# Optimization experiments

Measured on AMD Instinct MI355X. Metric: run time of the kernel, lower is better.

The kernel has to match this reference:

```python
import jax, jax.numpy as jnp
import numpy as np

DIM = 384
NUM_HEADS = 12
WS = 8            # window_size
SS = 4            # shift_size
HEAD_DIM = DIM // NUM_HEADS
SCALE = HEAD_DIM ** -0.5
N = WS * WS       # tokens per window
EPS = 1e-5
MLP_HIDDEN = 4 * DIM

# relative position index (static, matches torch buffer construction)
_coords = np.stack(np.meshgrid(np.arange(WS), np.arange(WS), indexing='ij')).reshape(2, -1)
_rel = (_coords[:, :, None] - _coords[:, None, :]).transpose(1, 2, 0)  # [N,N,2]
_rel[..., 0] += WS - 1
_rel[..., 1] += WS - 1
_rel[..., 0] *= 2 * WS - 1
RPI = jnp.asarray(_rel.sum(-1))  # [N,N] int


def layer_norm(x, g, b):
    m = x.mean(-1, keepdims=True)
    v = ((x - m) ** 2).mean(-1, keepdims=True)
    return (x - m) / jnp.sqrt(v + EPS) * g + b


def window_partition(x):
    B, Hh, Ww, C = x.shape
    x = x.reshape(B, Hh // WS, WS, Ww // WS, WS, C).transpose(0, 1, 3, 2, 4, 5)
    return x.reshape(-1, WS, WS, C)


def window_reverse(w, Hh, Ww):
    B = w.shape[0] // ((Hh // WS) * (Ww // WS))
    x = w.reshape(B, Hh // WS, Ww // WS, WS, WS, -1).transpose(0, 1, 3, 2, 4, 5)
    return x.reshape(B, Hh, Ww, -1)


def attention_mask(Hp, Wp):
    # region id along each axis: 0 = [0, Hp-WS), 1 = [Hp-WS, Hp-SS), 2 = [Hp-SS, Hp)
    h_id = np.zeros(Hp, np.int32); h_id[Hp - WS:Hp - SS] = 1; h_id[Hp - SS:] = 2
    w_id = np.zeros(Wp, np.int32); w_id[Wp - WS:Wp - SS] = 1; w_id[Wp - SS:] = 2
    cnt = h_id[:, None] * 3 + w_id[None, :]                      # [Hp, Wp]
    img = jnp.asarray(cnt, jnp.float32).reshape(1, Hp, Wp, 1)
    mw = window_partition(img).reshape(-1, N)                    # [nW, N]
    am = mw[:, None, :] - mw[:, :, None]                         # [nW, N, N]
    return jnp.where(am != 0, jnp.float32(-100.0), jnp.float32(0.0))


def setup_inputs() -> dict:
    key = jax.random.key(0)
    ks = jax.random.split(key, 8)
    B, H, W = 32, 64, 64
    std = 0.02
    return {
        'x': jax.random.normal(ks[0], (B, H * W, DIM), jnp.float32),
        'qkv_w': jax.random.normal(ks[1], (DIM, 3 * DIM), jnp.float32) * std,
        'qkv_b': jnp.zeros((3 * DIM,), jnp.float32),
        'proj_w': jax.random.normal(ks[2], (DIM, DIM), jnp.float32) * std,
        'proj_b': jnp.zeros((DIM,), jnp.float32),
        'rpb_table': jax.random.normal(ks[3], ((2 * WS - 1) * (2 * WS - 1), NUM_HEADS), jnp.float32) * std,
        'n1_g': jnp.ones((DIM,), jnp.float32), 'n1_b': jnp.zeros((DIM,), jnp.float32),
        'n2_g': jnp.ones((DIM,), jnp.float32), 'n2_b': jnp.zeros((DIM,), jnp.float32),
        'fc1_w': jax.random.normal(ks[4], (DIM, MLP_HIDDEN), jnp.float32) * std,
        'fc1_b': jnp.zeros((MLP_HIDDEN,), jnp.float32),
        'fc2_w': jax.random.normal(ks[5], (MLP_HIDDEN, DIM), jnp.float32) * std,
        'fc2_b': jnp.zeros((DIM,), jnp.float32),
        'H': 64, 'W': 64,
    }


def reference(x, qkv_w, qkv_b, proj_w, proj_b, rpb_table, n1_g, n1_b, n2_g, n2_b,
              fc1_w, fc1_b, fc2_w, fc2_b, H, W):
    B, L, C = x.shape
    shortcut = x
    h = layer_norm(x, n1_g, n1_b).reshape(B, H, W, C)
    pad_r = (WS - W % WS) % WS
    pad_b = (WS - H % WS) % WS
    if pad_r or pad_b:
        h = jnp.pad(h, ((0, 0), (0, pad_b), (0, pad_r), (0, 0)))
    Hp, Wp = H + pad_b, W + pad_r
    shifted = jnp.roll(h, shift=(-SS, -SS), axis=(1, 2))
    xw = window_partition(shifted).reshape(-1, N, C)             # [B_, N, C]
    B_ = xw.shape[0]

    qkv = (xw @ qkv_w + qkv_b).reshape(B_, N, 3, NUM_HEADS, HEAD_DIM)
    q = qkv[:, :, 0].transpose(0, 2, 1, 3) * SCALE               # [B_, h, N, d]
    k = qkv[:, :, 1].transpose(0, 2, 1, 3)
    v = qkv[:, :, 2].transpose(0, 2, 1, 3)

    attn = jnp.einsum('bhnd,bhmd->bhnm', q, k)                   # [B_, h, N, N]
    bias = rpb_table[RPI].transpose(2, 0, 1)                     # [h, N, N]
    attn = attn + bias[None]

    mask = attention_mask(Hp, Wp)                                # [nW, N, N]
    nW = mask.shape[0]
    attn = attn.reshape(B_ // nW, nW, NUM_HEADS, N, N) + mask[None, :, None]
    attn = jax.nn.softmax(attn.reshape(B_, NUM_HEADS, N, N), axis=-1)

    out = jnp.einsum('bhnm,bhmd->bhnd', attn, v)
    out = out.transpose(0, 2, 1, 3).reshape(B_, N, C)
    out = out @ proj_w + proj_b

    out = window_reverse(out.reshape(-1, WS, WS, C), Hp, Wp)
    out = jnp.roll(out, shift=(SS, SS), axis=(1, 2))
    out = out[:, :H, :W, :].reshape(B, H * W, C)

    x = shortcut + out
    h2 = layer_norm(x, n2_g, n2_b)
    mlp = jax.nn.gelu(h2 @ fc1_w + fc1_b, approximate=False) @ fc2_w + fc2_b
    return x + mlp
```

## Files before the change

### kernel.cpp

```cpp
#include <hip/hip_runtime.h>
#include <math.h>


#define ROWS_TOTAL 131072
#define NWIN_TOTAL 2048

typedef __attribute__((ext_vector_type(8))) __bf16 bf16x8;
typedef __attribute__((ext_vector_type(4))) float f32x4;
typedef __attribute__((ext_vector_type(8))) unsigned short ushort8;

__device__ __forceinline__ unsigned short f2bf(float f) {
  unsigned u = __builtin_bit_cast(unsigned, f);
  u = (u + 0x7fffu + ((u >> 16) & 1u)) >> 16;
  return (unsigned short)u;
}
__device__ __forceinline__ float bf2f(unsigned short u) {
  return __builtin_bit_cast(float, (unsigned)u << 16);
}

__device__ __forceinline__ void gload16(const void* g, void* l) {
  __builtin_amdgcn_global_load_lds(
      (const __attribute__((address_space(1))) unsigned int*)g,
      (__attribute__((address_space(3))) unsigned int*)l, 16, 0, 0);
}

__device__ __forceinline__ int gather_row(int win, int t) {
  int b = win >> 6, wi = (win >> 3) & 7, wj = win & 7;
  int gi = (wi * 8 + (t >> 3) + 4) & 63;
  int gj = (wj * 8 + (t & 7) + 4) & 63;
  return (b << 12) + (gi << 6) + gj;
}

__device__ __forceinline__ float gelu_f(float v) {
  float x = v * 0.70710678118654752f;
  float ax = fabsf(x);
  float t = 1.f / (1.f + 0.3275911f * ax);
  float poly =
      t * (0.254829592f +
           t * (-0.284496736f +
                t * (1.421413741f + t * (-1.453152027f + t * 1.061405429f))));
  float er = 1.f - poly * __expf(-x * x);
  er = copysignf(er, x);
  return 0.5f * v * (1.f + er);
}

#define LGK0() asm volatile("s_waitcnt lgkmcnt(0)" ::: "memory")
#define VM4() asm volatile("s_waitcnt vmcnt(4)" ::: "memory")
#define VM0() asm volatile("s_waitcnt vmcnt(0)" ::: "memory")
#define SCB() __builtin_amdgcn_sched_barrier(0)
#define BARR() __builtin_amdgcn_s_barrier()
#define PRIO1() __builtin_amdgcn_s_setprio(1)
#define PRIO0() __builtin_amdgcn_s_setprio(0)

#define STGA_(buf_, kt_, c_)                                          \
  gload16(aSrcC[c_] + (size_t)(kt_) * 64,                             \
          (char*)As + (buf_) * 32768 + (c_) * 8192 + w * 1024)
#define STGB_(buf_, kt_, c_)                                          \
  gload16(bSrcC[c_] + (size_t)(kt_) * 64,                             \
          (char*)Bs + (buf_) * 24576 + (c_) * 8192 + w * 1024)

#define MM3(mi_, a_, bs_)                                             \
  { acc[mi_][0] = __builtin_amdgcn_mfma_f32_16x16x32_bf16(            \
        a_, bs_[0], acc[mi_][0], 0, 0, 0);                            \
    acc[mi_][1] = __builtin_amdgcn_mfma_f32_16x16x32_bf16(            \
        a_, bs_[1], acc[mi_][1], 0, 0, 0);                            \
    acc[mi_][2] = __builtin_amdgcn_mfma_f32_16x16x32_bf16(            \
        a_, bs_[2], acc[mi_][2], 0, 0, 0); }

#define GEMM_DECLS()                                                  \
  f32x4 acc[8][3];                                                    \
  _Pragma("unroll") for (int i_ = 0; i_ < 8; ++i_)                    \
  _Pragma("unroll") for (int j_ = 0; j_ < 3; ++j_)                    \
      acc[i_][j_] = (f32x4)(0.f);                                     \
  const int sl0 = ((hi) ^ (lr & 7)) * 8;                              \
  const int sl1 = ((4 + hi) ^ (lr & 7)) * 8;                          \
  const int aB0 = (wr * 128 + lr) * 64 + sl0;                         \
  const int aB1 = (wr * 128 + lr) * 64 + sl1;                         \
  const int bB0 = (wc * 48 + lr) * 64 + sl0;                          \
  const int bB1 = (wc * 48 + lr) * 64 + sl1;

#define GEMM_CORE(NT_)                                                \
  {                                                                   \
    STGA_(0, 0, 0); STGA_(0, 0, 1); STGA_(0, 0, 2); STGA_(0, 0, 3);   \
    STGB_(0, 0, 0); STGB_(0, 0, 1); STGB_(0, 0, 2);                   \
    STGA_(1, 1, 0); STGA_(1, 1, 1); STGA_(1, 1, 2); STGA_(1, 1, 3);   \
    VM4(); SCB(); BARR(); SCB();                                      \
    int curA = 0;                                                     \
    for (int t = 0; t < (NT_); ++t) {                                 \
      const int curB = t & 1;                                         \
      const ushort* AsC = (const ushort*)As + curA * 16384;           \
      const ushort* BsC = (const ushort*)Bs + curB * 12288;           \
      if (t + 1 < (NT_)) {                                            \
        STGB_(curB ^ 1, t + 1, 0);                                    \
        STGB_(curB ^ 1, t + 1, 1);                                    \
        STGB_(curB ^ 1, t + 1, 2);                                    \
      }                                                               \
      SCB();                                                          \
      bf16x8 av0, av1, av2, av3, bv0[3], bv1[3];                      \
      bv0[0] = *(const bf16x8*)(BsC + bB0);                           \
      bv0[1] = *(const bf16x8*)(BsC + bB0 + 1024);                    \
      bv0[2] = *(const bf16x8*)(BsC + bB0 + 2048);                    \
      bv1[0] = *(const bf16x8*)(BsC + bB1);                           \
      bv1[1] = *(const bf16x8*)(BsC + bB1 + 1024);                    \
      bv1[2] = *(const bf16x8*)(BsC + bB1 + 2048);                    \
      av0 = *(const bf16x8*)(AsC + aB0);                              \
      av1 = *(const bf16x8*)(AsC + aB0 + 1024);                       \
      av2 = *(const bf16x8*)(AsC + aB0 + 2048);                       \
      av3 = *(const bf16x8*)(AsC + aB0 + 3072);                       \
      LGK0(); SCB();                                                  \
      PRIO1();                                                        \
      MM3(0, av0, bv0); MM3(1, av1, bv0);                             \
      MM3(2, av2, bv0); MM3(3, av3, bv0);                             \
      PRIO0(); SCB();                                                 \
      av0 = *(const bf16x8*)(AsC + aB1);                              \
      av1 = *(const bf16x8*)(AsC + aB1 + 1024);                       \
      av2 = *(const bf16x8*)(AsC + aB1 + 2048);                       \
      av3 = *(const bf16x8*)(AsC + aB1 + 3072);                       \
      LGK0(); SCB();                                                  \
      PRIO1();                                                        \
      MM3(0, av0, bv1); MM3(1, av1, bv1);                             \
      MM3(2, av2, bv1); MM3(3, av3, bv1);                             \
      PRIO0(); SCB();                                                 \
      if (t + 2 < (NT_)) {                                            \
        int nbA = curA + 2; if (nbA >= 3) nbA -= 3;                   \
        STGA_(nbA, t + 2, 0); STGA_(nbA, t + 2, 1);                   \
        STGA_(nbA, t + 2, 2); STGA_(nbA, t + 2, 3);                   \
      }                                                               \
      SCB();                                                          \
      av0 = *(const bf16x8*)(AsC + aB0 + 4096);                       \
      av1 = *(const bf16x8*)(AsC + aB0 + 5120);                       \
      av2 = *(const bf16x8*)(AsC + aB0 + 6144);                       \
      av3 = *(const bf16x8*)(AsC + aB0 + 7168);                       \
      LGK0(); SCB();                                                  \
      PRIO1();                                                        \
      MM3(4, av0, bv0); MM3(5, av1, bv0);                             \
      MM3(6, av2, bv0); MM3(7, av3, bv0);                             \
      PRIO0(); SCB();                                                 \
      av0 = *(const bf16x8*)(AsC + aB1 + 4096);                       \
      av1 = *(const bf16x8*)(AsC + aB1 + 5120);                       \
      av2 = *(const bf16x8*)(AsC + aB1 + 6144);                       \
      av3 = *(const bf16x8*)(AsC + aB1 + 7168);                       \
      LGK0(); SCB();                                                  \
      PRIO1();                                                        \
      MM3(4, av0, bv1); MM3(5, av1, bv1);                             \
      MM3(6, av2, bv1); MM3(7, av3, bv1);                             \
      PRIO0();                                                        \
      if (t + 2 < (NT_)) { VM4(); SCB(); BARR(); SCB(); }             \
      else if (t + 1 < (NT_)) { VM0(); SCB(); BARR(); SCB(); }        \
      ++curA; if (curA == 3) curA = 0;                                \
    }                                                                 \
  }

#define GRID_SWZ(NP_)                                                 \
  int p, bm;                                                          \
  {                                                                   \
    int lin = blockIdx.y * (NP_) + blockIdx.x;                        \
    if ((gridDim.y & 7) == 0) {                                       \
      int xcd = lin & 7, q = lin >> 3;                                \
      p = q % (NP_); bm = (q / (NP_)) * 8 + xcd;                      \
    } else { p = blockIdx.x; bm = blockIdx.y; }                       \
  }

__global__ __launch_bounds__(256) void wprep_k(
    const float* __restrict__ qkvw, const float* __restrict__ projw,
    const float* __restrict__ fc1w, const float* __restrict__ fc2w,
    ushort* __restrict__ wq, ushort* __restrict__ wp,
    ushort* __restrict__ w1, ushort* __restrict__ w2) {
  int gid = blockIdx.x * 256 + threadIdx.x;
  const int S1 = 1152 * 384;
  const int S2 = S1 + 384 * 384;
  const int S3 = S2 + 1536 * 384;
  const int S4 = S3 + 384 * 1536;
  if (gid < S1) {
    int n = gid / 384, k = gid - n * 384;
    wq[gid] = f2bf(qkvw[(size_t)k * 1152 + n]);
  } else if (gid < S2) {
    int i = gid - S1, n = i / 384, k = i - n * 384;
    wp[i] = f2bf(projw[(size_t)k * 384 + n]);
  } else if (gid < S3) {
    int i = gid - S2, n = i / 384, k = i - n * 384;
    w1[i] = f2bf(fc1w[(size_t)k * 1536 + n]);
  } else if (gid < S4) {
    int i = gid - S3, n = i / 1536, k = i - n * 1536;
    w2[i] = f2bf(fc2w[(size_t)k * 384 + n]);
  }
}

__global__ __launch_bounds__(256) void ln_fused_k(
    const float* __restrict__ x, const float* __restrict__ g,
    const float* __restrict__ b, ushort* __restrict__ o) {
  int wid = threadIdx.x >> 6, lane = threadIdx.x & 63;
  int row = (blockIdx.x << 2) + wid;
  const float* p = x + (size_t)row * 384;
  float2 v[3];
  float s = 0.f, ss = 0.f;
#pragma unroll
  for (int c = 0; c < 3; ++c) {
    v[c] = *(const float2*)(p + lane * 2 + c * 128);
    s += v[c].x + v[c].y;
    ss += v[c].x * v[c].x + v[c].y * v[c].y;
  }
#pragma unroll
  for (int off = 1; off < 64; off <<= 1) {
    s += __shfl_xor(s, off);
    ss += __shfl_xor(ss, off);
  }
  float m = s * (1.f / 384.f);
  float r = rsqrtf(ss * (1.f / 384.f) - m * m + 1e-5f);
  ushort* op = o + (size_t)row * 384;
#pragma unroll
  for (int c = 0; c < 3; ++c) {
    float2 gg = *(const float2*)(g + lane * 2 + c * 128);
    float2 bb = *(const float2*)(b + lane * 2 + c * 128);
    union { ushort u[2]; unsigned w; } pk;
    pk.u[0] = f2bf((v[c].x - m) * r * gg.x + bb.x);
    pk.u[1] = f2bf((v[c].y - m) * r * gg.y + bb.y);
    *(unsigned*)(op + lane * 2 + c * 128) = pk.w;
  }
}

__global__ __launch_bounds__(512) void qkv_mfma_k(
    const ushort* __restrict__ xln, const ushort* __restrict__ wq,
    const float* __restrict__ qkvb, ushort* __restrict__ qd,
    ushort* __restrict__ kd, ushort* __restrict__ vd, int wc0) {
  __shared__ __align__(16) ushort As[3][16384];
  __shared__ __align__(16) ushort Bs[2][12288];
  const int tid = threadIdx.x;
  const int w = tid >> 6, lane = tid & 63;
  const int wr = w >> 2, wc = w & 3;
  const int lr = lane & 15, hi = lane >> 4;
  GRID_SWZ(6);
  const int n0 = p * 192;
  const int sg = ((tid & 7) ^ ((tid >> 3) & 7)) * 8;
  const ushort* aSrcC[4];
  const ushort* bSrcC[3];
#pragma unroll
  for (int c = 0; c < 4; ++c)
    aSrcC[c] =
        xln + (size_t)gather_row(wc0 + bm * 4 + c, tid >> 3) * 384 + sg;
#pragma unroll
  for (int c = 0; c < 3; ++c)
    bSrcC[c] = wq + (size_t)(n0 + c * 64 + (tid >> 3)) * 384 + sg;
  GEMM_DECLS();
  GEMM_CORE(6);
  const float scale = 0.17677669529663687f;
#pragma unroll
  for (int mi = 0; mi < 8; ++mi) {
#pragma unroll
    for (int r = 0; r < 4; ++r) {
      int rr = wr * 128 + mi * 16 + (hi << 2) + r;
      int w_rel = bm * 4 + (rr >> 6), t = rr & 63;
#pragma unroll
      for (int nj = 0; nj < 3; ++nj) {
        int nc = n0 + wc * 48 + nj * 16 + lr;
        float v = acc[mi][nj][r] + qkvb[nc];
        int qi = nc / 384, rem = nc - qi * 384;
        int hh = rem >> 5, d = rem & 31;
        ushort* base = (qi == 0) ? qd : (qi == 1 ? kd : vd);
        if (qi == 0) v *= scale;
        base[(((size_t)w_rel * 12 + hh) << 11) + (t << 5) + d] = f2bf(v);
      }
    }
  }
}

__global__ __launch_bounds__(128) void attn_k(
    const ushort* __restrict__ q, const ushort* __restrict__ k,
    const ushort* __restrict__ v, const float* __restrict__ rpb,
    ushort* __restrict__ ao, int wc0) {
  __shared__ __align__(16) float kbuf[2][64][32];
  __shared__ __align__(16) float vbuf[2][64][32];
  __shared__ float bias[2][232];
  __shared__ int region[64];
  const int tid = threadIdx.x;
  const int wid = tid >> 6, lane = tid & 63;
  const int w = blockIdx.x, win = wc0 + w;
  const int head = blockIdx.y * 2 + wid;
  if (tid < 64) {
    int wi = (win >> 3) & 7, wj = win & 7;
    int pi = wi * 8 + (tid >> 3), pj = wj * 8 + (tid & 7);
    int ri = pi < 56 ? 0 : (pi < 60 ? 1 : 2);
    int rj = pj < 56 ? 0 : (pj < 60 ? 1 : 2);
    region[tid] = ri * 3 + rj;
  }
  const size_t hb = ((size_t)w * 12 + head) * 2048;
  const ushort* kp = k + hb;
  const ushort* vp = v + hb;
#pragma unroll
  for (int s = 0; s < 4; ++s) {
    int f = s * 64 + lane;
    int r = f >> 2, c = (f & 3) * 8;
    ushort8 ku = *(const ushort8*)(kp + r * 32 + c);
    ushort8 vu = *(const ushort8*)(vp + r * 32 + c);
#pragma unroll
    for (int j = 0; j < 8; ++j) {
      kbuf[wid][r][c + j] = bf2f(ku[j]);
      vbuf[wid][r][c + j] = bf2f(vu[j]);
    }
  }
  for (int s = lane; s < 225; s += 64) bias[wid][s] = rpb[s * 12 + head];
  __syncthreads();
  const int i = lane;
  float qr[32];
  const ushort* qp = q + hb + (i << 5);
#pragma unroll
  for (int c = 0; c < 4; ++c) {
    ushort8 qu = *(const ushort8*)(qp + c * 8);
#pragma unroll
    for (int j = 0; j < 8; ++j) qr[c * 8 + j] = bf2f(qu[j]);
  }
  const int yi = i >> 3, xi = i & 7, regi = region[i];
  float sc[64];
  float mx = -3.0e38f;
#pragma unroll
  for (int j = 0; j < 64; ++j) {
    float a = 0.f;
#pragma unroll
    for (int c = 0; c < 32; c += 4) {
      float4 kv = *(float4*)&kbuf[wid][j][c];
      a = fmaf(qr[c], kv.x, a);
      a = fmaf(qr[c + 1], kv.y, a);
      a = fmaf(qr[c + 2], kv.z, a);
      a = fmaf(qr[c + 3], kv.w, a);
    }
    int dy = yi - (j >> 3) + 7, dx = xi - (j & 7) + 7;
    a += bias[wid][dy * 15 + dx];
    if (region[j] != regi) a -= 100.f;
    sc[j] = a;
    mx = fmaxf(mx, a);
  }
  float sum = 0.f;
#pragma unroll
  for (int j = 0; j < 64; ++j) {
    float e = __expf(sc[j] - mx);
    sc[j] = e;
    sum += e;
  }
  const float inv = 1.f / sum;
  float o[32];
#pragma unroll
  for (int c = 0; c < 32; ++c) o[c] = 0.f;
#pragma unroll
  for (int j = 0; j < 64; ++j) {
    float p = sc[j];
#pragma unroll
    for (int c = 0; c < 32; c += 4) {
      float4 vv = *(float4*)&vbuf[wid][j][c];
      o[c] = fmaf(p, vv.x, o[c]);
      o[c + 1] = fmaf(p, vv.y, o[c + 1]);
      o[c + 2] = fmaf(p, vv.z, o[c + 2]);
      o[c + 3] = fmaf(p, vv.w, o[c + 3]);
    }
  }
  ushort* op = ao + ((size_t)(w * 64 + i)) * 384 + (head << 5);
#pragma unroll
  for (int c = 0; c < 32; c += 8) {
    ushort8 pk;
#pragma unroll
    for (int j2 = 0; j2 < 8; ++j2) pk[j2] = f2bf(o[c + j2] * inv);
    *(ushort8*)(op + c) = pk;
  }
}

__global__ __launch_bounds__(512) void proj_mfma_k(
    const ushort* __restrict__ ao, const ushort* __restrict__ wp,
    const float* __restrict__ pb, const float* __restrict__ x,
    float* __restrict__ x2, int wc0) {
  __shared__ __align__(16) ushort As[3][16384];
  __shared__ __align__(16) ushort Bs[2][12288];
  const int tid = threadIdx.x;
  const int w = tid >> 6, lane = tid & 63;
  const int wr = w >> 2, wc = w & 3;
  const int lr = lane & 15, hi = lane >> 4;
  GRID_SWZ(2);
  const int n0 = p * 192;
  const int sg = ((tid & 7) ^ ((tid >> 3) & 7)) * 8;
  const ushort* aSrcC[4];
  const ushort* bSrcC[3];
#pragma unroll
  for (int c = 0; c < 4; ++c)
    aSrcC[c] = ao + (size_t)(bm * 256 + c * 64 + (tid >> 3)) * 384 + sg;
#pragma unroll
  for (int c = 0; c < 3; ++c)
    bSrcC[c] = wp + (size_t)(n0 + c * 64 + (tid >> 3)) * 384 + sg;
  GEMM_DECLS();
  GEMM_CORE(6);
#pragma unroll
  for (int mi = 0; mi < 8; ++mi) {
#pragma unroll
    for (int r = 0; r < 4; ++r) {
      int rr = wr * 128 + mi * 16 + (hi << 2) + r;
      int gl = bm * 256 + rr;
      int gr = gather_row(wc0 + (gl >> 6), gl & 63);
#pragma unroll
      for (int nj = 0; nj < 3; ++nj) {
        int nc = n0 + wc * 48 + nj * 16 + lr;
        size_t idx = (size_t)gr * 384 + nc;
        x2[idx] = acc[mi][nj][r] + pb[nc] + x[idx];
      }
    }
  }
}

__global__ __launch_bounds__(512) void fc1_mfma_k(
    const ushort* __restrict__ x2ln, const ushort* __restrict__ w1,
    const float* __restrict__ fb, ushort* __restrict__ hm, int row0) {
  __shared__ __align__(16) ushort As[3][16384];
  __shared__ __align__(16) ushort Bs[2][12288];
  const int tid = threadIdx.x;
  const int w = tid >> 6, lane = tid & 63;
  const int wr = w >> 2, wc = w & 3;
  const int lr = lane & 15, hi = lane >> 4;
  GRID_SWZ(8);
  const int n0 = p * 192;
  const int sg = ((tid & 7) ^ ((tid >> 3) & 7)) * 8;
  const ushort* aSrcC[4];
  const ushort* bSrcC[3];
#pragma unroll
  for (int c = 0; c < 4; ++c)
    aSrcC[c] =
        x2ln + (size_t)(row0 + bm * 256 + c * 64 + (tid >> 3)) * 384 + sg;
#pragma unroll
  for (int c = 0; c < 3; ++c)
    bSrcC[c] = w1 + (size_t)(n0 + c * 64 + (tid >> 3)) * 384 + sg;
  GEMM_DECLS();
  GEMM_CORE(6);
#pragma unroll
  for (int mi = 0; mi < 8; ++mi) {
#pragma unroll
    for (int r = 0; r < 4; ++r) {
      int rr = wr * 128 + mi * 16 + (hi << 2) + r;
      size_t lrow = (size_t)(bm * 256 + rr);
#pragma unroll
      for (int nj = 0; nj < 3; ++nj) {
        int nc = n0 + wc * 48 + nj * 16 + lr;
        float v = gelu_f(acc[mi][nj][r] + fb[nc]);
        hm[lrow * 1536 + nc] = f2bf(v);
      }
    }
  }
}

__global__ __launch_bounds__(512) void fc2_mfma_k(
    const ushort* __restrict__ hm, const ushort* __restrict__ w2,
    const float* __restrict__ fb, float* __restrict__ out, int row0) {
  __shared__ __align__(16) ushort As[3][16384];
  __shared__ __align__(16) ushort Bs[2][12288];
  const int tid = threadIdx.x;
  const int w = tid >> 6, lane = tid & 63;
  const int wr = w >> 2, wc = w & 3;
  const int lr = lane & 15, hi = lane >> 4;
  GRID_SWZ(2);
  const int n0 = p * 192;
  const int sg = ((tid & 7) ^ ((tid >> 3) & 7)) * 8;
  const ushort* aSrcC[4];
  const ushort* bSrcC[3];
#pragma unroll
  for (int c = 0; c < 4; ++c)
    aSrcC[c] = hm + (size_t)(bm * 256 + c * 64 + (tid >> 3)) * 1536 + sg;
#pragma unroll
  for (int c = 0; c < 3; ++c)
    bSrcC[c] = w2 + (size_t)(n0 + c * 64 + (tid >> 3)) * 1536 + sg;
  GEMM_DECLS();
  GEMM_CORE(24);
#pragma unroll
  for (int mi = 0; mi < 8; ++mi) {
#pragma unroll
    for (int r = 0; r < 4; ++r) {
      int rr = wr * 128 + mi * 16 + (hi << 2) + r;
      size_t grow = (size_t)(row0 + bm * 256 + rr);
#pragma unroll
      for (int nj = 0; nj < 3; ++nj) {
        int nc = n0 + wc * 48 + nj * 16 + lr;
        size_t idx = grow * 384 + nc;
        out[idx] = out[idx] + acc[mi][nj][r] + fb[nc];
      }
    }
  }
}

extern "C" void kernel_launch(void* const* d_in, const int* in_sizes, int n_in,
                              void* d_out, int out_size, void* d_ws, size_t ws_size,
                              hipStream_t stream) {
  const float* x = (const float*)d_in[0];
  const float* qkv_w = (const float*)d_in[1];
  const float* qkv_b = (const float*)d_in[2];
  const float* proj_w = (const float*)d_in[3];
  const float* proj_b = (const float*)d_in[4];
  const float* rpb = (const float*)d_in[5];
  const float* n1g = (const float*)d_in[6];
  const float* n1b = (const float*)d_in[7];
  const float* n2g = (const float*)d_in[8];
  const float* n2b = (const float*)d_in[9];
  const float* fc1w = (const float*)d_in[10];
  const float* fc1b = (const float*)d_in[11];
  const float* fc2w = (const float*)d_in[12];
  const float* fc2b = (const float*)d_in[13];
  float* out = (float*)d_out;
  char* ws = (char*)d_ws;

  ushort* wq = (ushort*)ws;
  ushort* wp = wq + 442368;
  ushort* w1 = wp + 147456;
  ushort* w2 = w1 + 589824;
  ushort* xln = (ushort*)(ws + 3538944);
  char* scratch = ws + 3538944 + 100663296;
  size_t base = 3538944 + 100663296;
  size_t ssz = (ws_size > base) ? ws_size - base : 0;

  wprep_k<<<6912, 256, 0, stream>>>(qkv_w, proj_w, fc1w, fc2w, wq, wp, w1, w2);
  ln_fused_k<<<ROWS_TOTAL / 4, 256, 0, stream>>>(x, n1g, n1b, xln);

  const size_t perwin = 196608;
  int nwc = (int)(ssz / perwin);
  if (nwc > NWIN_TOTAL) nwc = NWIN_TOTAL;
  nwc &= ~31;
  if (nwc < 32) nwc = 32;
  ushort* qd = (ushort*)scratch;
  ushort* kd = qd + (size_t)nwc * 24576;
  ushort* vd = kd + (size_t)nwc * 24576;
  ushort* ao = vd + (size_t)nwc * 24576;
  for (int wc0 = 0; wc0 < NWIN_TOTAL; wc0 += nwc) {
    int nw = (NWIN_TOTAL - wc0 < nwc) ? (NWIN_TOTAL - wc0) : nwc;
    qkv_mfma_k<<<dim3(6, nw / 4), 512, 0, stream>>>(xln, wq, qkv_b, qd, kd,
                                                    vd, wc0);
    attn_k<<<dim3(nw, 6), 128, 0, stream>>>(qd, kd, vd, rpb, ao, wc0);
    proj_mfma_k<<<dim3(2, nw / 4), 512, 0, stream>>>(ao, wp, proj_b, x, out,
                                                     wc0);
  }

  ln_fused_k<<<ROWS_TOTAL / 4, 256, 0, stream>>>(out, n2g, n2b, xln);
  const size_t pergrp = 786432;
  int ngc = (int)(ssz / pergrp);
  if (ngc > 512) ngc = 512;
  ngc &= ~7;
  if (ngc < 8) ngc = 8;
  ushort* hm = (ushort*)scratch;
  for (int g0 = 0; g0 < 512; g0 += ngc) {
    int ng = (512 - g0 < ngc) ? (512 - g0) : ngc;
    fc1_mfma_k<<<dim3(8, ng), 512, 0, stream>>>(xln, w1, fc1b, hm, g0 * 256);
    fc2_mfma_k<<<dim3(2, ng), 512, 0, stream>>>(hm, w2, fc2b, out, g0 * 256);
  }
}
```

Baseline: 1.373 ms.

## Simplify GEMM inner loop, pack QKV row-major, cap chunk sizes, add launch bounds

The hand-scheduled GEMM inner loop, with its sched barriers, priority switches and explicit lgkmcnt waits, is replaced by plain unrolled loops, leaving instruction scheduling to the compiler. The QKV output is stored as one row-major [rows,1152] buffer, and attention reads K, V and Q by strided column offsets instead of separate per-head contiguous arrays. Window and MLP group chunk caps shrink to 256 and 128 so intermediates stay more cache-resident, and the GEMM kernels get launch_bounds(512,2) to target two blocks per CU. These changes risk losing the tuned LDS/MFMA overlap and make attention loads less coalesced, while the occupancy hint may force register spills.

```diff
diff --git a/kernel.cpp b/kernel.cpp
--- a/kernel.cpp
+++ b/kernel.cpp
@@ -44,13 +44,9 @@
   return 0.5f * v * (1.f + er);
 }
 
-#define LGK0() asm volatile("s_waitcnt lgkmcnt(0)" ::: "memory")
 #define VM4() asm volatile("s_waitcnt vmcnt(4)" ::: "memory")
 #define VM0() asm volatile("s_waitcnt vmcnt(0)" ::: "memory")
-#define SCB() __builtin_amdgcn_sched_barrier(0)
-#define BARR() __builtin_amdgcn_s_barrier()
-#define PRIO1() __builtin_amdgcn_s_setprio(1)
-#define PRIO0() __builtin_amdgcn_s_setprio(0)
+#define ABAR() asm volatile("s_barrier" ::: "memory")
 
 #define STGA_(buf_, kt_, c_)                                          \
   gload16(aSrcC[c_] + (size_t)(kt_) * 64,                             \
@@ -58,14 +54,6 @@
 #define STGB_(buf_, kt_, c_)                                          \
   gload16(bSrcC[c_] + (size_t)(kt_) * 64,                             \
           (char*)Bs + (buf_) * 24576 + (c_) * 8192 + w * 1024)
-
-#define MM3(mi_, a_, bs_)                                             \
-  { acc[mi_][0] = __builtin_amdgcn_mfma_f32_16x16x32_bf16(            \
-        a_, bs_[0], acc[mi_][0], 0, 0, 0);                            \
-    acc[mi_][1] = __builtin_amdgcn_mfma_f32_16x16x32_bf16(            \
-        a_, bs_[1], acc[mi_][1], 0, 0, 0);                            \
-    acc[mi_][2] = __builtin_amdgcn_mfma_f32_16x16x32_bf16(            \
-        a_, bs_[2], acc[mi_][2], 0, 0, 0); }
 
 #define GEMM_DECLS()                                                  \
   f32x4 acc[8][3];                                                    \
@@ -84,7 +72,7 @@
     STGA_(0, 0, 0); STGA_(0, 0, 1); STGA_(0, 0, 2); STGA_(0, 0, 3);   \
     STGB_(0, 0, 0); STGB_(0, 0, 1); STGB_(0, 0, 2);                   \
     STGA_(1, 1, 0); STGA_(1, 1, 1); STGA_(1, 1, 2); STGA_(1, 1, 3);   \
-    VM4(); SCB(); BARR(); SCB();                                      \
+    VM4(); ABAR();                                                    \
     int curA = 0;                                                     \
     for (int t = 0; t < (NT_); ++t) {                                 \
       const int curB = t & 1;                                         \
@@ -95,58 +83,28 @@
         STGB_(curB ^ 1, t + 1, 1);                                    \
         STGB_(curB ^ 1, t + 1, 2);                                    \
       }                                                               \
-      SCB();                                                          \
-      bf16x8 av0, av1, av2, av3, bv0[3], bv1[3];                      \
-      bv0[0] = *(const bf16x8*)(BsC + bB0);                           \
-      bv0[1] = *(const bf16x8*)(BsC + bB0 + 1024);                    \
-      bv0[2] = *(const bf16x8*)(BsC + bB0 + 2048);                    \
-      bv1[0] = *(const bf16x8*)(BsC + bB1);                           \
-      bv1[1] = *(const bf16x8*)(BsC + bB1 + 1024);                    \
-      bv1[2] = *(const bf16x8*)(BsC + bB1 + 2048);                    \
-      av0 = *(const bf16x8*)(AsC + aB0);                              \
-      av1 = *(const bf16x8*)(AsC + aB0 + 1024);                       \
-      av2 = *(const bf16x8*)(AsC + aB0 + 2048);                       \
-      av3 = *(const bf16x8*)(AsC + aB0 + 3072);                       \
-      LGK0(); SCB();                                                  \
-      PRIO1();                                                        \
-      MM3(0, av0, bv0); MM3(1, av1, bv0);                             \
-      MM3(2, av2, bv0); MM3(3, av3, bv0);                             \
-      PRIO0(); SCB();                                                 \
-      av0 = *(const bf16x8*)(AsC + aB1);                              \
-      av1 = *(const bf16x8*)(AsC + aB1 + 1024);                       \
-      av2 = *(const bf16x8*)(AsC + aB1 + 2048);                       \
-      av3 = *(const bf16x8*)(AsC + aB1 + 3072);                       \
-      LGK0(); SCB();                                                  \
-      PRIO1();                                                        \
-      MM3(0, av0, bv1); MM3(1, av1, bv1);                             \
-      MM3(2, av2, bv1); MM3(3, av3, bv1);                             \
-      PRIO0(); SCB();                                                 \
       if (t + 2 < (NT_)) {                                            \
         int nbA = curA + 2; if (nbA >= 3) nbA -= 3;                   \
         STGA_(nbA, t + 2, 0); STGA_(nbA, t + 2, 1);                   \
         STGA_(nbA, t + 2, 2); STGA_(nbA, t + 2, 3);                   \
       }                                                               \
-      SCB();                                                          \
-      av0 = *(const bf16x8*)(AsC + aB0 + 4096);                       \
-      av1 = *(const bf16x8*)(AsC + aB0 + 5120);                       \
-      av2 = *(const bf16x8*)(AsC + aB0 + 6144);                       \
-      av3 = *(const bf16x8*)(AsC + aB0 + 7168);                       \
-      LGK0(); SCB();                                                  \
-      PRIO1();                                                        \
-      MM3(4, av0, bv0); MM3(5, av1, bv0);                             \
-      MM3(6, av2, bv0); MM3(7, av3, bv0);                             \
-      PRIO0(); SCB();                                                 \
-      av0 = *(const bf16x8*)(AsC + aB1 + 4096);                       \
-      av1 = *(const bf16x8*)(AsC + aB1 + 5120);                       \
-      av2 = *(const bf16x8*)(AsC + aB1 + 6144);                       \
-      av3 = *(const bf16x8*)(AsC + aB1 + 7168);                       \
-      LGK0(); SCB();                                                  \
-      PRIO1();                                                        \
-      MM3(4, av0, bv1); MM3(5, av1, bv1);                             \
-      MM3(6, av2, bv1); MM3(7, av3, bv1);                             \
-      PRIO0();                                                        \
-      if (t + 2 < (NT_)) { VM4(); SCB(); BARR(); SCB(); }             \
-      else if (t + 1 < (NT_)) { VM0(); SCB(); BARR(); SCB(); }        \
+      bf16x8 bv0[3], bv1[3];                                          \
+      _Pragma("unroll") for (int nj = 0; nj < 3; ++nj) {              \
+        bv0[nj] = *(const bf16x8*)(BsC + bB0 + nj * 1024);            \
+        bv1[nj] = *(const bf16x8*)(BsC + bB1 + nj * 1024);            \
+      }                                                               \
+      _Pragma("unroll") for (int mi = 0; mi < 8; ++mi) {              \
+        bf16x8 a0 = *(const bf16x8*)(AsC + aB0 + mi * 1024);          \
+        bf16x8 a1 = *(const bf16x8*)(AsC + aB1 + mi * 1024);          \
+        _Pragma("unroll") for (int nj = 0; nj < 3; ++nj) {            \
+          acc[mi][nj] = __builtin_amdgcn_mfma_f32_16x16x32_bf16(      \
+              a0, bv0[nj], acc[mi][nj], 0, 0, 0);                     \
+          acc[mi][nj] = __builtin_amdgcn_mfma_f32_16x16x32_bf16(      \
+              a1, bv1[nj], acc[mi][nj], 0, 0, 0);                     \
+        }                                                             \
+      }                                                               \
+      if (t + 2 < (NT_)) { VM4(); ABAR(); }                           \
+      else if (t + 1 < (NT_)) { VM0(); ABAR(); }                      \
       ++curA; if (curA == 3) curA = 0;                                \
     }                                                                 \
   }
@@ -219,10 +177,9 @@
   }
 }
 
-__global__ __launch_bounds__(512) void qkv_mfma_k(
+__global__ __launch_bounds__(512, 2) void qkv_mfma_k(
     const ushort* __restrict__ xln, const ushort* __restrict__ wq,
-    const float* __restrict__ qkvb, ushort* __restrict__ qd,
-    ushort* __restrict__ kd, ushort* __restrict__ vd, int wc0) {
+    const float* __restrict__ qkvb, ushort* __restrict__ qkvd, int wc0) {
   __shared__ __align__(16) ushort As[3][16384];
   __shared__ __align__(16) ushort Bs[2][12288];
   const int tid = threadIdx.x;
@@ -249,24 +206,20 @@
 #pragma unroll
     for (int r = 0; r < 4; ++r) {
       int rr = wr * 128 + mi * 16 + (hi << 2) + r;
-      int w_rel = bm * 4 + (rr >> 6), t = rr & 63;
+      size_t row = (size_t)(bm * 256 + rr);
 #pragma unroll
       for (int nj = 0; nj < 3; ++nj) {
         int nc = n0 + wc * 48 + nj * 16 + lr;
         float v = acc[mi][nj][r] + qkvb[nc];
-        int qi = nc / 384, rem = nc - qi * 384;
-        int hh = rem >> 5, d = rem & 31;
-        ushort* base = (qi == 0) ? qd : (qi == 1 ? kd : vd);
-        if (qi == 0) v *= scale;
-        base[(((size_t)w_rel * 12 + hh) << 11) + (t << 5) + d] = f2bf(v);
+        if (nc < 384) v *= scale;
+        qkvd[row * 1152 + nc] = f2bf(v);
       }
     }
   }
 }
 
 __global__ __launch_bounds__(128) void attn_k(
-    const ushort* __restrict__ q, const ushort* __restrict__ k,
-    const ushort* __restrict__ v, const float* __restrict__ rpb,
+    const ushort* __restrict__ qkv, const float* __restrict__ rpb,
     ushort* __restrict__ ao, int wc0) {
   __shared__ __align__(16) float kbuf[2][64][32];
   __shared__ __align__(16) float vbuf[2][64][32];
@@ -283,15 +236,14 @@
     int rj = pj < 56 ? 0 : (pj < 60 ? 1 : 2);
     region[tid] = ri * 3 + rj;
   }
-  const size_t hb = ((size_t)w * 12 + head) * 2048;
-  const ushort* kp = k + hb;
-  const ushort* vp = v + hb;
+  const ushort* base = qkv + (size_t)(w * 64) * 1152;
+  const int kcol = 384 + head * 32, vcol = 768 + head * 32;
 #pragma unroll
   for (int s = 0; s < 4; ++s) {
     int f = s * 64 + lane;
     int r = f >> 2, c = (f & 3) * 8;
-    ushort8 ku = *(const ushort8*)(kp + r * 32 + c);
-    ushort8 vu = *(const ushort8*)(vp + r * 32 + c);
+    ushort8 ku = *(const ushort8*)(base + (size_t)r * 1152 + kcol + c);
+    ushort8 vu = *(const ushort8*)(base + (size_t)r * 1152 + vcol + c);
 #pragma unroll
     for (int j = 0; j < 8; ++j) {
       kbuf[wid][r][c + j] = bf2f(ku[j]);
@@ -302,7 +254,7 @@
   __syncthreads();
   const int i = lane;
   float qr[32];
-  const ushort* qp = q + hb + (i << 5);
+  const ushort* qp = base + (size_t)i * 1152 + head * 32;
 #pragma unroll
   for (int c = 0; c < 4; ++c) {
     ushort8 qu = *(const ushort8*)(qp + c * 8);
@@ -362,7 +314,7 @@
   }
 }
 
-__global__ __launch_bounds__(512) void proj_mfma_k(
+__global__ __launch_bounds__(512, 2) void proj_mfma_k(
     const ushort* __restrict__ ao, const ushort* __restrict__ wp,
     const float* __restrict__ pb, const float* __restrict__ x,
     float* __restrict__ x2, int wc0) {
@@ -402,7 +354,7 @@
   }
 }
 
-__global__ __launch_bounds__(512) void fc1_mfma_k(
+__global__ __launch_bounds__(512, 2) void fc1_mfma_k(
     const ushort* __restrict__ x2ln, const ushort* __restrict__ w1,
     const float* __restrict__ fb, ushort* __restrict__ hm, int row0) {
   __shared__ __align__(16) ushort As[3][16384];
@@ -441,7 +393,7 @@
   }
 }
 
-__global__ __launch_bounds__(512) void fc2_mfma_k(
+__global__ __launch_bounds__(512, 2) void fc2_mfma_k(
     const ushort* __restrict__ hm, const ushort* __restrict__ w2,
     const float* __restrict__ fb, float* __restrict__ out, int row0) {
   __shared__ __align__(16) ushort As[3][16384];
@@ -513,18 +465,15 @@
 
   const size_t perwin = 196608;
   int nwc = (int)(ssz / perwin);
-  if (nwc > NWIN_TOTAL) nwc = NWIN_TOTAL;
+  if (nwc > 256) nwc = 256;
   nwc &= ~31;
   if (nwc < 32) nwc = 32;
-  ushort* qd = (ushort*)scratch;
-  ushort* kd = qd + (size_t)nwc * 24576;
-  ushort* vd = kd + (size_t)nwc * 24576;
-  ushort* ao = vd + (size_t)nwc * 24576;
+  ushort* qkvd = (ushort*)scratch;
+  ushort* ao = qkvd + (size_t)nwc * 73728;
   for (int wc0 = 0; wc0 < NWIN_TOTAL; wc0 += nwc) {
     int nw = (NWIN_TOTAL - wc0 < nwc) ? (NWIN_TOTAL - wc0) : nwc;
-    qkv_mfma_k<<<dim3(6, nw / 4), 512, 0, stream>>>(xln, wq, qkv_b, qd, kd,
-                                                    vd, wc0);
-    attn_k<<<dim3(nw, 6), 128, 0, stream>>>(qd, kd, vd, rpb, ao, wc0);
+    qkv_mfma_k<<<dim3(6, nw / 4), 512, 0, stream>>>(xln, wq, qkv_b, qkvd, wc0);
+    attn_k<<<dim3(nw, 6), 128, 0, stream>>>(qkvd, rpb, ao, wc0);
     proj_mfma_k<<<dim3(2, nw / 4), 512, 0, stream>>>(ao, wp, proj_b, x, out,
                                                      wc0);
   }
@@ -532,7 +481,7 @@
   ln_fused_k<<<ROWS_TOTAL / 4, 256, 0, stream>>>(out, n2g, n2b, xln);
   const size_t pergrp = 786432;
   int ngc = (int)(ssz / pergrp);
-  if (ngc > 512) ngc = 512;
+  if (ngc > 128) ngc = 128;
   ngc &= ~7;
   if (ngc < 8) ngc = 8;
   ushort* hm = (ushort*)scratch;
```

Result: slower. 1.903 ms (+38.6%).
